# Kernel tuning notes

Measured on AMD Instinct MI355X. Metric: run time of the kernel, lower is better.

## Reference

```python
import jax, jax.numpy as jnp
import numpy as np

N, D, R, L, E, EP = 50000, 256, 16, 2, 300000, 100000
SCALING = 16.0 / 16.0  # alpha / rank


def _ln(x, g, b, eps=1e-5):
    mu = x.mean(-1, keepdims=True)
    var = ((x - mu) ** 2).mean(-1, keepdims=True)
    return (x - mu) * jax.lax.rsqrt(var + eps) * g + b


def setup_inputs() -> dict:
    key = jax.random.key(0)
    ks = iter(jax.random.split(key, 32))
    f = lambda shp, s=0.05: jax.random.normal(next(ks), shp, jnp.float32) * s
    return dict(
        x=f((2, N, D), 1.0),
        W_in=f((2, D, D)), b_in=f((2, D)),
        lora_A=f((2, R, D)), lora_B=f((2, D, R), 0.01),
        pn_g=jnp.ones((2, D), jnp.float32), pn_b=jnp.zeros((2, D), jnp.float32),
        W_self=f((L, 2, D, D)), W_neigh=f((L, 2, D, D)), b_sage=f((L, 2, D)),
        ln_g=jnp.ones((L, 2, D), jnp.float32), ln_b=jnp.zeros((L, 2, D), jnp.float32),
        Wv=f((2, D, D)), bv=f((2, D)), Wo=f((2, D, D)), bo=f((2, D)),
        e_src=jax.random.randint(next(ks), (2, E), 0, N, jnp.int32),
        e_dst=jax.random.randint(next(ks), (2, E), 0, N, jnp.int32),
        pos_src=jax.random.randint(next(ks), (EP,), 0, N, jnp.int32),
        pos_dst=jax.random.randint(next(ks), (EP,), 0, N, jnp.int32),
        neg_src=jax.random.randint(next(ks), (EP,), 0, N, jnp.int32),
        neg_dst=jax.random.randint(next(ks), (EP,), 0, N, jnp.int32),
    )


def reference(x, W_in, b_in, lora_A, lora_B, pn_g, pn_b, W_self, W_neigh,
              b_sage, ln_g, ln_b, Wv, bv, Wo, bo,
              e_src, e_dst, pos_src, pos_dst, neg_src, neg_dst):
    # ---- per-type input projection + LoRA adapter + patient LayerNorm ----
    base = jnp.einsum('tnd,tod->tno', x, W_in) + b_in[:, None]
    ad = jnp.einsum('tnr,tdr->tnd', jnp.einsum('tnd,trd->tnr', x, lora_A), lora_B) * SCALING
    h = _ln(base + ad, pn_g[:, None], pn_b[:, None])  # [2, N, D]

    def seg_mean(v, i):  # mean aggregation over incoming edges
        s = jax.ops.segment_sum(v, i, num_segments=N)
        c = jax.ops.segment_sum(jnp.ones((i.shape[0], 1), v.dtype), i, num_segments=N)
        return s / jnp.maximum(c, 1.0)

    # ---- SAGE layers over blocks (relation 0: a->b, relation 1: b->a) ----
    for i in range(L):
        msgs = jax.vmap(lambda hr, sr: hr[sr])(h, e_src)      # [2, E, D], src type r
        agg = jax.vmap(seg_mean)(msgs, e_dst)                 # agg[r] lands at dst type 1-r
        neigh = agg[::-1]                                     # neigh[t] for node type t
        h_new = (jnp.einsum('tnd,tod->tno', h, W_self[i])
                 + jnp.einsum('tnd,tod->tno', neigh, W_neigh[i])
                 + b_sage[i][:, None])
        if i == L - 1:
            # nn.MultiheadAttention with seq_len=1: softmax over 1 key == 1,
            # so attn_out = out_proj(v_proj(x)).
            v = jnp.einsum('tnd,tod->tno', h_new, Wv) + bv[:, None]
            h_new = jnp.einsum('tnd,tod->tno', v, Wo) + bo[:, None]
        if i > 0:
            h_new = h_new + h  # residual (shapes always match)
        h = _ln(h_new, ln_g[i][:, None], ln_b[i][:, None])
        # dropout is identity at inference

    # ---- dot-product edge predictor on pos/neg graphs for etype (a, rel, b) ----
    h_a, h_b = h[0], h[1]
    pos_score = jnp.sum(h_a[pos_src] * h_b[pos_dst], axis=-1)
    neg_score = jnp.sum(h_a[neg_src] * h_b[neg_dst], axis=-1)
    return pos_score, neg_score
```

## Files before the change

kernel.cpp:

```cpp
#include <hip/hip_runtime.h>

#define D 256
#define BK 64
#define SCAN_NB 64
#define SCAN_T (SCAN_NB * 256)

typedef __attribute__((ext_vector_type(8))) short bf16x8;
typedef __attribute__((ext_vector_type(4))) float f32x4;
typedef __attribute__((ext_vector_type(4))) unsigned int u32x4;

union frag_cvt { u32x4 u; bf16x8 h; };

__device__ __forceinline__ unsigned short bf16_rn(float f) {
    const unsigned int u = __float_as_uint(f);
    return (unsigned short)((u + 0x7FFFu + ((u >> 16) & 1u)) >> 16);
}
__device__ __forceinline__ float bf16_to_f32(unsigned short s) {
    return __uint_as_float(((unsigned int)s) << 16);
}

__global__ __launch_bounds__(256) void pre1_kernel(
    const float* __restrict__ W_in, const float* __restrict__ lA, const float* __restrict__ lB,
    unsigned short* __restrict__ win_eff,
    const float* __restrict__ W_self, unsigned short* __restrict__ ws0,
    const float* __restrict__ W_neigh, unsigned short* __restrict__ wn0,
    const float* __restrict__ Wo, const float* __restrict__ Wv, float* __restrict__ wvo,
    const float* __restrict__ bvp, const float* __restrict__ bo, float* __restrict__ bvo)
{
    const int b = blockIdx.x, tid = threadIdx.x;
    if (b < 512) {
        const int t = b >> 8, o = b & 255;
        float acc = W_in[((size_t)t * D + o) * D + tid];
        const float* Br = lB + ((size_t)t * D + o) * 16;
        const float* At = lA + (size_t)t * 16 * D;
        #pragma unroll
        for (int r = 0; r < 16; ++r) acc = fmaf(Br[r], At[r * D + tid], acc);
        win_eff[((size_t)t * D + o) * D + tid] = bf16_rn(acc);
    } else if (b < 1024) {
        const int i = (b - 512) * 256 + tid;
        ws0[i] = bf16_rn(W_self[i]);
    } else if (b < 1536) {
        const int i = (b - 1024) * 256 + tid;
        wn0[i] = bf16_rn(W_neigh[i]);
    } else if (b < 2048) {
        const int t = (b - 1536) >> 8, p = (b - 1536) & 255;
        const float* Xr = Wo + ((size_t)t * D + p) * D;
        const float* Yt = Wv + (size_t)t * D * D;
        float acc = 0.f;
        for (int o = 0; o < D; ++o) acc = fmaf(Xr[o], Yt[(size_t)o * D + tid], acc);
        wvo[((size_t)t * D + p) * D + tid] = acc;
    } else {
        const int t = b - 2048;
        const float* Mr = Wo + ((size_t)t * D + tid) * D;
        const float* vr = bvp + (size_t)t * D;
        float acc = bo[(size_t)t * D + tid];
        for (int o = 0; o < D; ++o) acc = fmaf(Mr[o], vr[o], acc);
        bvo[(size_t)t * D + tid] = acc;
    }
}

__global__ __launch_bounds__(256) void pre2_kernel(
    const float* __restrict__ wvo,
    const float* __restrict__ W_self1, unsigned short* __restrict__ ws1,
    const float* __restrict__ W_neigh1, unsigned short* __restrict__ wn1,
    const float* __restrict__ b_sage1, const float* __restrict__ bvo, float* __restrict__ b1e)
{
    const int b = blockIdx.x, tid = threadIdx.x;
    if (b < 512) {
        const int t = b >> 8, p = b & 255;
        const float* Xr = wvo + ((size_t)t * D + p) * D;
        const float* Yt = W_self1 + (size_t)t * D * D;
        float acc = 0.f;
        for (int o = 0; o < D; ++o) acc = fmaf(Xr[o], Yt[(size_t)o * D + tid], acc);
        ws1[((size_t)t * D + p) * D + tid] = bf16_rn(acc);
    } else if (b < 1024) {
        const int t = (b - 512) >> 8, p = (b - 512) & 255;
        const float* Xr = wvo + ((size_t)t * D + p) * D;
        const float* Yt = W_neigh1 + (size_t)t * D * D;
        float acc = 0.f;
        for (int o = 0; o < D; ++o) acc = fmaf(Xr[o], Yt[(size_t)o * D + tid], acc);
        wn1[((size_t)t * D + p) * D + tid] = bf16_rn(acc);
    } else {
        const int t = b - 1024;
        const float* Mr = wvo + ((size_t)t * D + tid) * D;
        const float* vr = b_sage1 + (size_t)t * D;
        float acc = bvo[(size_t)t * D + tid];
        for (int o = 0; o < D; ++o) acc = fmaf(Mr[o], vr[o], acc);
        b1e[(size_t)t * D + tid] = acc;
    }
}

__device__ __forceinline__ void load_bfrag(const unsigned short* __restrict__ Wp,
                                           int wn, int cidx, int rgrp,
                                           int kh, bf16x8 (&bq)[4][4])
{
    #pragma unroll
    for (int n = 0; n < 4; ++n) {
        const int o = wn + n * 16 + cidx;
        #pragma unroll
        for (int kk = 0; kk < 4; ++kk) {
            frag_cvt c;
            c.u = *(const u32x4*)(Wp + (size_t)o * D + kh * 128 + kk * 32 + rgrp * 8);
            bq[n][kk] = c.h;
        }
    }
}

__device__ __forceinline__ void gload_tile64(const unsigned short* __restrict__ Abase,
                                             int r0, int kt, int tid, char* lbuf)
{
    const int wbase = (tid >> 6) << 10;
    #pragma unroll
    for (int c = 0; c < 2; ++c) {
        const int p   = c * 4096 + tid * 16;
        const int row = p >> 7;
        const int lwb = p & 127;
        const int lg  = lwb ^ ((row & 7) << 4);
        const unsigned short* g = Abase + (size_t)(r0 + row) * D + kt + (lg >> 1);
        char* l = lbuf + c * 4096 + wbase;
        __builtin_amdgcn_global_load_lds(
            (const __attribute__((address_space(1))) unsigned int*)g,
            (__attribute__((address_space(3))) unsigned int*)l, 16, 0, 0);
    }
}

__device__ __forceinline__ void ln_epilogue(
    f32x4 (&acc)[4][4], unsigned short* SH,
    const float* __restrict__ bias, const unsigned short* __restrict__ res_bf,
    const float* __restrict__ g, const float* __restrict__ b,
    unsigned short* __restrict__ out_bf,
    int t, int m0, int M, int tid, int wid, int rgrp, int cidx, int wn)
{
    #pragma unroll
    for (int n = 0; n < 4; ++n) {
        const float bc = bias[t * D + wn + n * 16 + cidx];
        #pragma unroll
        for (int m = 0; m < 4; ++m)
            #pragma unroll
            for (int i = 0; i < 4; ++i)
                acc[m][n][i] += bc;
    }
    if (res_bf) {
        #pragma unroll
        for (int m = 0; m < 4; ++m)
            #pragma unroll
            for (int i = 0; i < 4; ++i) {
                const int row = m * 16 + rgrp * 4 + i;
                const int gr  = min(m0 + row, M - 1);
                const unsigned short* rr = res_bf + ((size_t)t * M + gr) * D + wn + cidx;
                #pragma unroll
                for (int n = 0; n < 4; ++n)
                    acc[m][n][i] += bf16_to_f32(rr[n * 16]);
            }
    }
    float* red  = (float*)((char*)SH + 16384);
    float* red2 = red + 256;
    float mu[4][4], rs[4][4];
    #pragma unroll
    for (int m = 0; m < 4; ++m)
        #pragma unroll
        for (int i = 0; i < 4; ++i) {
            float s = 0.f;
            #pragma unroll
            for (int n = 0; n < 4; ++n) s += acc[m][n][i];
            s += __shfl_xor(s, 1); s += __shfl_xor(s, 2);
            s += __shfl_xor(s, 4); s += __shfl_xor(s, 8);
            if (cidx == 0) red[(m * 16 + rgrp * 4 + i) * 4 + wid] = s;
        }
    __syncthreads();
    #pragma unroll
    for (int m = 0; m < 4; ++m)
        #pragma unroll
        for (int i = 0; i < 4; ++i) {
            const int row = m * 16 + rgrp * 4 + i;
            mu[m][i] = (red[row * 4] + red[row * 4 + 1] +
                        red[row * 4 + 2] + red[row * 4 + 3]) * (1.0f / 256.0f);
            float q = 0.f;
            #pragma unroll
            for (int n = 0; n < 4; ++n) {
                const float d0 = acc[m][n][i] - mu[m][i];
                q += d0 * d0;
            }
            q += __shfl_xor(q, 1); q += __shfl_xor(q, 2);
            q += __shfl_xor(q, 4); q += __shfl_xor(q, 8);
            if (cidx == 0) red2[row * 4 + wid] = q;
        }
    __syncthreads();
    #pragma unroll
    for (int m = 0; m < 4; ++m)
        #pragma unroll
        for (int i = 0; i < 4; ++i) {
            const int row = m * 16 + rgrp * 4 + i;
            rs[m][i] = rsqrtf((red2[row * 4] + red2[row * 4 + 1] +
                               red2[row * 4 + 2] + red2[row * 4 + 3]) * (1.0f / 256.0f) + 1e-5f);
        }
    __syncthreads();
    #pragma unroll
    for (int n = 0; n < 4; ++n) {
        const int col = wn + n * 16 + cidx;
        const float gv = g[t * D + col];
        const float bv = b[t * D + col];
        #pragma unroll
        for (int m = 0; m < 4; ++m)
            #pragma unroll
            for (int i = 0; i < 4; ++i) {
                const int row = m * 16 + rgrp * 4 + i;
                SH[row * 264 + col] = bf16_rn((acc[m][n][i] - mu[m][i]) * rs[m][i] * gv + bv);
            }
    }
    __syncthreads();
    unsigned short* Ct = out_bf + (size_t)t * M * D;
    #pragma unroll
    for (int it = 0; it < 8; ++it) {
        const int gidx = tid + it * 256;
        const int row  = gidx >> 5;
        const int cg   = gidx & 31;
        const int grow = m0 + row;
        if (grow < M) {
            const u32x4 v = *(const u32x4*)&SH[row * 264 + cg * 8];
            *(u32x4*)(Ct + (size_t)grow * D + cg * 8) = v;
        }
    }
}

__global__ __launch_bounds__(256, 2) void gemm_ln_kernel(
    const unsigned short* __restrict__ A, const unsigned short* __restrict__ W1,
    const unsigned short* __restrict__ A2, const unsigned short* __restrict__ W2,
    const float* __restrict__ bias, const unsigned short* __restrict__ res_bf,
    const float* __restrict__ g, const float* __restrict__ b,
    unsigned short* __restrict__ out_bf, int M, int swap2)
{
    const int t   = blockIdx.z;
    const int m0  = blockIdx.x * 64;
    const int tid = threadIdx.x;
    const int lane = tid & 63;
    const int wid  = tid >> 6;
    const int wn = wid * 64;
    const int rgrp = lane >> 4;
    const int cidx = lane & 15;

    __shared__ __align__(16) unsigned short SH[64 * 264];
    char* AsB0 = (char*)SH;
    char* AsB1 = (char*)SH + 8192;

    const int t2 = swap2 ? (1 - t) : t;
    const unsigned short* Aps[2] = { A  + (size_t)t  * M * D, A2 + (size_t)t2 * M * D };
    const unsigned short* Wps[2] = { W1 + (size_t)t  * D * D, W2 + (size_t)t  * D * D };

    f32x4 acc[4][4];
    #pragma unroll
    for (int i = 0; i < 4; ++i)
        #pragma unroll
        for (int j = 0; j < 4; ++j)
            acc[i][j] = (f32x4){0.f, 0.f, 0.f, 0.f};

    bf16x8 bq[2][4][4];
    gload_tile64(Aps[0], m0, 0, tid, AsB0);
    load_bfrag(Wps[0], wn, cidx, rgrp, 0, bq[0]);

    #pragma unroll
    for (int idx = 0; idx < 8; ++idx) {
        __syncthreads();
        if (idx < 7)
            gload_tile64(Aps[(idx + 1) >> 2], m0, ((idx + 1) & 3) * BK, tid,
                         (idx & 1) ? AsB0 : AsB1);
        if ((idx & 1) == 1 && idx < 7) {
            const int nh = (idx >> 1) + 1;
            load_bfrag(Wps[nh >> 1], wn, cidx, rgrp, nh & 1, bq[nh & 1]);
        }
        const char* cb = (idx & 1) ? AsB1 : AsB0;
        const int half = idx >> 1;
        #pragma unroll
        for (int ks = 0; ks < 2; ++ks) {
            const int kb = ks * 64 + rgrp * 16;
            bf16x8 af[4];
            #pragma unroll
            for (int m = 0; m < 4; ++m) {
                const int row = m * 16 + cidx;
                const int sw  = (row * 128 + kb) ^ ((row & 7) << 4);
                frag_cvt c; c.u = *(const u32x4*)(cb + sw); af[m] = c.h;
            }
            #pragma unroll
            for (int m = 0; m < 4; ++m)
                #pragma unroll
                for (int n = 0; n < 4; ++n)
                    acc[m][n] = __builtin_amdgcn_mfma_f32_16x16x32_bf16(
                        af[m], bq[half & 1][n][(idx & 1) * 2 + ks], acc[m][n], 0, 0, 0);
        }
        __syncthreads();
    }

    ln_epilogue(acc, SH, bias, res_bf, g, b, out_bf, t, m0, M, tid, wid, rgrp, cidx, wn);
}

__global__ __launch_bounds__(256, 2) void gemm_ln_in_kernel(
    const float* __restrict__ X, const unsigned short* __restrict__ Wb,
    const float* __restrict__ bias,
    const float* __restrict__ g, const float* __restrict__ b,
    unsigned short* __restrict__ out_bf, int M)
{
    const int t   = blockIdx.z;
    const int m0  = blockIdx.x * 64;
    const int tid = threadIdx.x;
    const int lane = tid & 63;
    const int wid  = tid >> 6;
    const int wn = wid * 64;
    const int rgrp = lane >> 4;
    const int cidx = lane & 15;

    __shared__ __align__(16) unsigned short SH[64 * 264];
    char* AsB = (char*)SH;

    const float* Xp = X + (size_t)t * M * D;
    const unsigned short* Wp = Wb + (size_t)t * D * D;

    f32x4 acc[4][4];
    #pragma unroll
    for (int i = 0; i < 4; ++i)
        #pragma unroll
        for (int j = 0; j < 4; ++j)
            acc[i][j] = (f32x4){0.f, 0.f, 0.f, 0.f};

    bf16x8 bq[2][4][4];
    float4 xr0[2], xr1[2];
    #pragma unroll
    for (int it = 0; it < 2; ++it) {
        const int gi = tid + it * 256;
        const int row = gi >> 3;
        const int kg = gi & 7;
        const int ar = min(m0 + row, M - 1);
        xr0[it] = *(const float4*)(Xp + (size_t)ar * D + kg * 8);
        xr1[it] = *(const float4*)(Xp + (size_t)ar * D + kg * 8 + 4);
    }
    load_bfrag(Wp, wn, cidx, rgrp, 0, bq[0]);

    #pragma unroll
    for (int kt_i = 0; kt_i < 4; ++kt_i) {
        #pragma unroll
        for (int it = 0; it < 2; ++it) {
            const int gi = tid + it * 256;
            const int row = gi >> 3;
            const int kg = gi & 7;
            unsigned int w[4];
            w[0] = ((unsigned int)bf16_rn(xr0[it].y) << 16) | bf16_rn(xr0[it].x);
            w[1] = ((unsigned int)bf16_rn(xr0[it].w) << 16) | bf16_rn(xr0[it].z);
            w[2] = ((unsigned int)bf16_rn(xr1[it].y) << 16) | bf16_rn(xr1[it].x);
            w[3] = ((unsigned int)bf16_rn(xr1[it].w) << 16) | bf16_rn(xr1[it].z);
            const int sw = ((row * BK + kg * 8) * 2) ^ ((row & 7) << 4);
            *(u32x4*)(AsB + sw) = (u32x4){w[0], w[1], w[2], w[3]};
        }
        __syncthreads();
        if (kt_i < 3) {
            const int kt = (kt_i + 1) * BK;
            #pragma unroll
            for (int it = 0; it < 2; ++it) {
                const int gi = tid + it * 256;
                const int row = gi >> 3;
                const int kg = gi & 7;
                const int ar = min(m0 + row, M - 1);
                xr0[it] = *(const float4*)(Xp + (size_t)ar * D + kt + kg * 8);
                xr1[it] = *(const float4*)(Xp + (size_t)ar * D + kt + kg * 8 + 4);
            }
        }
        if (kt_i == 1) load_bfrag(Wp, wn, cidx, rgrp, 1, bq[1]);
        #pragma unroll
        for (int ks = 0; ks < 2; ++ks) {
            const int kb = ks * 64 + rgrp * 16;
            bf16x8 af[4];
            #pragma unroll
            for (int m = 0; m < 4; ++m) {
                const int row = m * 16 + cidx;
                const int sw  = (row * 128 + kb) ^ ((row & 7) << 4);
                frag_cvt c; c.u = *(u32x4*)(AsB + sw); af[m] = c.h;
            }
            #pragma unroll
            for (int m = 0; m < 4; ++m)
                #pragma unroll
                for (int n = 0; n < 4; ++n)
                    acc[m][n] = __builtin_amdgcn_mfma_f32_16x16x32_bf16(
                        af[m], bq[kt_i >> 1][n][(kt_i & 1) * 2 + ks], acc[m][n], 0, 0, 0);
        }
        __syncthreads();
    }

    ln_epilogue(acc, SH, bias, nullptr, g, b, out_bf, t, m0, M, tid, wid, rgrp, cidx, wn);
}

__global__ void count_kernel(const int* __restrict__ e_dst, int* __restrict__ cnt,
                             int E2, int N, int E)
{
    const int i = blockIdx.x * 256 + threadIdx.x;
    if (i >= E2) return;
    const int t = i / E;
    atomicAdd(&cnt[(size_t)t * N + e_dst[i]], 1);
}

__global__ __launch_bounds__(256) void scan1_kernel(const int* __restrict__ cnt,
                                                    int* __restrict__ texcl,
                                                    int* __restrict__ bsum, int n, int c)
{
    __shared__ int ts[256];
    const int tid = threadIdx.x;
    const int gt  = blockIdx.x * 256 + tid;
    const int b   = gt * c;
    const int e   = min(b + c, n);
    int s = 0;
    for (int i = b; i < e; ++i) s += cnt[i];
    ts[tid] = s;
    __syncthreads();
    #pragma unroll
    for (int off = 1; off < 256; off <<= 1) {
        const int v = (tid >= off) ? ts[tid - off] : 0;
        __syncthreads();
        ts[tid] += v;
        __syncthreads();
    }
    texcl[gt] = ts[tid] - s;
    if (tid == 255) bsum[blockIdx.x] = ts[255];
}

__global__ __launch_bounds__(64) void scan2_kernel(int* __restrict__ bsum,
                                                   int* __restrict__ bbase,
                                                   int* __restrict__ offs, int n, int nb)
{
    const int lane = threadIdx.x;
    int v = (lane < nb) ? bsum[lane] : 0;
    int s = v;
    #pragma unroll
    for (int off = 1; off < 64; off <<= 1) {
        const int u = __shfl_up(s, off);
        if (lane >= off) s += u;
    }
    if (lane < nb) bbase[lane] = s - v;
    if (lane == 63) offs[n] = s;
}

__global__ __launch_bounds__(256) void scan3_kernel(const int* __restrict__ cnt,
                                                    const int* __restrict__ texcl,
                                                    const int* __restrict__ bbase,
                                                    int* __restrict__ offs, int n, int c)
{
    const int tid = threadIdx.x;
    const int gt  = blockIdx.x * 256 + tid;
    const int b   = gt * c;
    const int e   = min(b + c, n);
    int base = bbase[blockIdx.x] + texcl[gt];
    for (int i = b; i < e; ++i) { offs[i] = base; base += cnt[i]; }
}

__global__ void fill_kernel(const int* __restrict__ e_src, const int* __restrict__ e_dst,
                            const int* __restrict__ offs, int* __restrict__ cur,
                            int* __restrict__ sorted, int E2, int N, int E)
{
    const int i = blockIdx.x * 256 + threadIdx.x;
    if (i >= E2) return;
    const int t = i / E;
    const int idx = t * N + e_dst[i];
    const int pos = offs[idx] + atomicAdd(&cur[idx], 1);
    sorted[pos] = e_src[i];
}

__global__ __launch_bounds__(256) void agg_kernel(
    const unsigned short* __restrict__ hbf, const int* __restrict__ sorted_src,
    const int* __restrict__ offs, unsigned short* __restrict__ aggbf, int N)
{
    const int gw   = (blockIdx.x * 256 + threadIdx.x) >> 6;
    const int lane = threadIdx.x & 63;
    if (gw >= 2 * N) return;
    const int t = (gw >= N) ? 1 : 0;
    const int beg = offs[gw];
    const int end = offs[gw + 1];
    const unsigned short* hb = hbf + (size_t)t * N * D;
    float4 a0 = make_float4(0.f, 0.f, 0.f, 0.f);
    float4 a1 = make_float4(0.f, 0.f, 0.f, 0.f);
    int e = beg;
    for (; e + 2 <= end; e += 2) {
        const int s0 = sorted_src[e];
        const int s1 = sorted_src[e + 1];
        const ushort4 v0 = *(const ushort4*)(hb + (size_t)s0 * D + lane * 4);
        const ushort4 v1 = *(const ushort4*)(hb + (size_t)s1 * D + lane * 4);
        a0.x += bf16_to_f32(v0.x); a0.y += bf16_to_f32(v0.y);
        a0.z += bf16_to_f32(v0.z); a0.w += bf16_to_f32(v0.w);
        a1.x += bf16_to_f32(v1.x); a1.y += bf16_to_f32(v1.y);
        a1.z += bf16_to_f32(v1.z); a1.w += bf16_to_f32(v1.w);
    }
    if (e < end) {
        const int s0 = sorted_src[e];
        const ushort4 v0 = *(const ushort4*)(hb + (size_t)s0 * D + lane * 4);
        a0.x += bf16_to_f32(v0.x); a0.y += bf16_to_f32(v0.y);
        a0.z += bf16_to_f32(v0.z); a0.w += bf16_to_f32(v0.w);
    }
    const float inv = 1.0f / fmaxf((float)(end - beg), 1.0f);
    ushort4 o;
    o.x = bf16_rn((a0.x + a1.x) * inv); o.y = bf16_rn((a0.y + a1.y) * inv);
    o.z = bf16_rn((a0.z + a1.z) * inv); o.w = bf16_rn((a0.w + a1.w) * inv);
    *(ushort4*)(aggbf + (size_t)gw * D + lane * 4) = o;
}

__global__ __launch_bounds__(256) void score_kernel(
    const unsigned short* __restrict__ h,
    const int* __restrict__ pos_src, const int* __restrict__ pos_dst,
    const int* __restrict__ neg_src, const int* __restrict__ neg_dst,
    float* __restrict__ out, int EP, int N)
{
    const int wid  = (blockIdx.x * 256 + threadIdx.x) >> 6;
    const int lane = threadIdx.x & 63;
    if (wid >= 2 * EP) return;
    const int kind = wid / EP;
    const int k    = wid - kind * EP;
    const int s = kind ? neg_src[k] : pos_src[k];
    const int d = kind ? neg_dst[k] : pos_dst[k];
    const ushort4 a = *(const ushort4*)(h + (size_t)s * D + lane * 4);
    const ushort4 b = *(const ushort4*)(h + ((size_t)N + d) * D + lane * 4);
    float v = bf16_to_f32(a.x) * bf16_to_f32(b.x)
            + bf16_to_f32(a.y) * bf16_to_f32(b.y)
            + bf16_to_f32(a.z) * bf16_to_f32(b.z)
            + bf16_to_f32(a.w) * bf16_to_f32(b.w);
    #pragma unroll
    for (int off = 32; off > 0; off >>= 1) v += __shfl_down(v, off);
    if (lane == 0) out[wid] = v;
}

extern "C" void kernel_launch(void* const* d_in, const int* in_sizes, int n_in,
                              void* d_out, int out_size, void* d_ws, size_t ws_size,
                              hipStream_t stream)
{
    const float* x      = (const float*)d_in[0];
    const float* W_in   = (const float*)d_in[1];
    const float* b_in   = (const float*)d_in[2];
    const float* lora_A = (const float*)d_in[3];
    const float* lora_B = (const float*)d_in[4];
    const float* pn_g   = (const float*)d_in[5];
    const float* pn_b   = (const float*)d_in[6];
    const float* W_self = (const float*)d_in[7];
    const float* W_neigh= (const float*)d_in[8];
    const float* b_sage = (const float*)d_in[9];
    const float* ln_g   = (const float*)d_in[10];
    const float* ln_b   = (const float*)d_in[11];
    const float* Wv     = (const float*)d_in[12];
    const float* bvp    = (const float*)d_in[13];
    const float* Wo     = (const float*)d_in[14];
    const float* bo     = (const float*)d_in[15];
    const int* e_src    = (const int*)d_in[16];
    const int* e_dst    = (const int*)d_in[17];
    const int* pos_src  = (const int*)d_in[18];
    const int* pos_dst  = (const int*)d_in[19];
    const int* neg_src  = (const int*)d_in[20];
    const int* neg_dst  = (const int*)d_in[21];

    const int N  = in_sizes[0] / (2 * D);
    const int E  = in_sizes[16] / 2;
    const int EP = in_sizes[18];
    const size_t ND2 = (size_t)2 * N * D;
    const size_t DD2 = (size_t)2 * D * D;
    const int n2 = 2 * N;

    unsigned short* P0 = (unsigned short*)d_ws;
    unsigned short* P1 = P0 + ND2;
    unsigned short* P2 = P1 + ND2;
    unsigned short* T  = P2 + ND2;
    int* cnt    = (int*)(T + ND2);
    int* cur    = cnt + (size_t)n2;
    int* offs   = cur + (size_t)n2;
    int* sorted = offs + (size_t)n2 + 1;
    int* texcl  = sorted + (size_t)2 * E;
    int* bsum   = texcl + SCAN_T;
    int* bbase  = bsum + SCAN_NB;
    float* wvo  = (float*)(bbase + SCAN_NB);
    float* bvo  = wvo + DD2;
    float* b1e  = bvo + 2 * D;
    unsigned short* win_eff = (unsigned short*)(b1e + 2 * D);
    unsigned short* ws0 = win_eff + DD2;
    unsigned short* wn0 = ws0 + DD2;
    unsigned short* ws1 = wn0 + DD2;
    unsigned short* wn1 = ws1 + DD2;

    pre1_kernel<<<2050, 256, 0, stream>>>(W_in, lora_A, lora_B, win_eff,
                                          W_self, ws0, W_neigh, wn0,
                                          Wo, Wv, wvo, bvp, bo, bvo);
    pre2_kernel<<<1026, 256, 0, stream>>>(wvo, W_self + DD2, ws1,
                                          W_neigh + DD2, wn1,
                                          b_sage + 2 * D, bvo, b1e);

    hipMemsetAsync(cnt, 0, (size_t)2 * n2 * sizeof(int), stream);
    count_kernel<<<(2 * E + 255) / 256, 256, 0, stream>>>(e_dst, cnt, 2 * E, N, E);
    const int sc = (n2 + SCAN_T - 1) / SCAN_T;
    scan1_kernel<<<SCAN_NB, 256, 0, stream>>>(cnt, texcl, bsum, n2, sc);
    scan2_kernel<<<1, 64, 0, stream>>>(bsum, bbase, offs, n2, SCAN_NB);
    scan3_kernel<<<SCAN_NB, 256, 0, stream>>>(cnt, texcl, bbase, offs, n2, sc);
    fill_kernel<<<(2 * E + 255) / 256, 256, 0, stream>>>(e_src, e_dst, offs, cur, sorted, 2 * E, N, E);

    const dim3 gblk(256);
    const int mpan = (N + 63) / 64;
    const dim3 fgrid(mpan, 1, 2);

    gemm_ln_in_kernel<<<fgrid, gblk, 0, stream>>>(x, win_eff, b_in, pn_g, pn_b, P0, N);

    agg_kernel<<<dim3((2 * N + 3) / 4, 1, 1), gblk, 0, stream>>>(P0, sorted, offs, P1, N);
    gemm_ln_kernel<<<fgrid, gblk, 0, stream>>>(P0, ws0, P1, wn0, b_sage, nullptr,
                                               ln_g, ln_b, P2, N, 1);

    agg_kernel<<<dim3((2 * N + 3) / 4, 1, 1), gblk, 0, stream>>>(P2, sorted, offs, P1, N);
    gemm_ln_kernel<<<fgrid, gblk, 0, stream>>>(P2, ws1, P1, wn1, b1e, P2,
                                               ln_g + 2 * D, ln_b + 2 * D, P0, N, 1);

    score_kernel<<<(2 * EP + 3) / 4, gblk, 0, stream>>>(P0, pos_src, pos_dst, neg_src, neg_dst,
                                                        (float*)d_out, EP, N);
}
```

Before: 466.5 us.

## Single-pass LayerNorm stats, 4-way unrolled aggregation, half-wave score dot products

Three independent changes. The LayerNorm epilogue of gemm_ln_kernel now computes sum and sum of squares in one pass, which removes a shuffle round and one block barrier at the cost of the less stable E[x^2]-mu^2 variance form, clamped at zero. The neighbour aggregation loop is unrolled 4-way with four accumulators to keep more gathers in flight. The score kernel now handles two edge pairs per wavefront using 16-byte loads per lane, halving the grid size.

```diff
diff --git a/kernel.cpp b/kernel.cpp
--- a/kernel.cpp
+++ b/kernel.cpp
@@ -160,12 +160,21 @@
     for (int m = 0; m < 4; ++m)
         #pragma unroll
         for (int i = 0; i < 4; ++i) {
-            float s = 0.f;
-            #pragma unroll
-            for (int n = 0; n < 4; ++n) s += acc[m][n][i];
-            s += __shfl_xor(s, 1); s += __shfl_xor(s, 2);
-            s += __shfl_xor(s, 4); s += __shfl_xor(s, 8);
-            if (cidx == 0) red[(m * 16 + rgrp * 4 + i) * 4 + wid] = s;
+            float s = 0.f, q = 0.f;
+            #pragma unroll
+            for (int n = 0; n < 4; ++n) {
+                const float v = acc[m][n][i];
+                s += v; q += v * v;
+            }
+            s += __shfl_xor(s, 1); q += __shfl_xor(q, 1);
+            s += __shfl_xor(s, 2); q += __shfl_xor(q, 2);
+            s += __shfl_xor(s, 4); q += __shfl_xor(q, 4);
+            s += __shfl_xor(s, 8); q += __shfl_xor(q, 8);
+            if (cidx == 0) {
+                const int row = m * 16 + rgrp * 4 + i;
+                red[row * 4 + wid]  = s;
+                red2[row * 4 + wid] = q;
+            }
         }
     __syncthreads();
     #pragma unroll
@@ -173,26 +182,13 @@
         #pragma unroll
         for (int i = 0; i < 4; ++i) {
             const int row = m * 16 + rgrp * 4 + i;
-            mu[m][i] = (red[row * 4] + red[row * 4 + 1] +
-                        red[row * 4 + 2] + red[row * 4 + 3]) * (1.0f / 256.0f);
-            float q = 0.f;
-            #pragma unroll
-            for (int n = 0; n < 4; ++n) {
-                const float d0 = acc[m][n][i] - mu[m][i];
-                q += d0 * d0;
-            }
-            q += __shfl_xor(q, 1); q += __shfl_xor(q, 2);
-            q += __shfl_xor(q, 4); q += __shfl_xor(q, 8);
-            if (cidx == 0) red2[row * 4 + wid] = q;
-        }
-    __syncthreads();
-    #pragma unroll
-    for (int m = 0; m < 4; ++m)
-        #pragma unroll
-        for (int i = 0; i < 4; ++i) {
-            const int row = m * 16 + rgrp * 4 + i;
-            rs[m][i] = rsqrtf((red2[row * 4] + red2[row * 4 + 1] +
-                               red2[row * 4 + 2] + red2[row * 4 + 3]) * (1.0f / 256.0f) + 1e-5f);
+            const float S = red[row * 4] + red[row * 4 + 1] + red[row * 4 + 2] + red[row * 4 + 3];
+            const float Q = red2[row * 4] + red2[row * 4 + 1] + red2[row * 4 + 2] + red2[row * 4 + 3];
+            const float m_ = S * (1.0f / 256.0f);
+            float var = Q * (1.0f / 256.0f) - m_ * m_;
+            var = fmaxf(var, 0.f);
+            mu[m][i] = m_;
+            rs[m][i] = rsqrtf(var + 1e-5f);
         }
     __syncthreads();
     #pragma unroll
@@ -473,18 +469,28 @@
     const unsigned short* hb = hbf + (size_t)t * N * D;
     float4 a0 = make_float4(0.f, 0.f, 0.f, 0.f);
     float4 a1 = make_float4(0.f, 0.f, 0.f, 0.f);
+    float4 a2 = make_float4(0.f, 0.f, 0.f, 0.f);
+    float4 a3 = make_float4(0.f, 0.f, 0.f, 0.f);
     int e = beg;
-    for (; e + 2 <= end; e += 2) {
+    for (; e + 4 <= end; e += 4) {
         const int s0 = sorted_src[e];
         const int s1 = sorted_src[e + 1];
+        const int s2 = sorted_src[e + 2];
+        const int s3 = sorted_src[e + 3];
         const ushort4 v0 = *(const ushort4*)(hb + (size_t)s0 * D + lane * 4);
         const ushort4 v1 = *(const ushort4*)(hb + (size_t)s1 * D + lane * 4);
+        const ushort4 v2 = *(const ushort4*)(hb + (size_t)s2 * D + lane * 4);
+        const ushort4 v3 = *(const ushort4*)(hb + (size_t)s3 * D + lane * 4);
         a0.x += bf16_to_f32(v0.x); a0.y += bf16_to_f32(v0.y);
         a0.z += bf16_to_f32(v0.z); a0.w += bf16_to_f32(v0.w);
         a1.x += bf16_to_f32(v1.x); a1.y += bf16_to_f32(v1.y);
         a1.z += bf16_to_f32(v1.z); a1.w += bf16_to_f32(v1.w);
-    }
-    if (e < end) {
+        a2.x += bf16_to_f32(v2.x); a2.y += bf16_to_f32(v2.y);
+        a2.z += bf16_to_f32(v2.z); a2.w += bf16_to_f32(v2.w);
+        a3.x += bf16_to_f32(v3.x); a3.y += bf16_to_f32(v3.y);
+        a3.z += bf16_to_f32(v3.z); a3.w += bf16_to_f32(v3.w);
+    }
+    for (; e < end; ++e) {
         const int s0 = sorted_src[e];
         const ushort4 v0 = *(const ushort4*)(hb + (size_t)s0 * D + lane * 4);
         a0.x += bf16_to_f32(v0.x); a0.y += bf16_to_f32(v0.y);
@@ -492,8 +498,10 @@
     }
     const float inv = 1.0f / fmaxf((float)(end - beg), 1.0f);
     ushort4 o;
-    o.x = bf16_rn((a0.x + a1.x) * inv); o.y = bf16_rn((a0.y + a1.y) * inv);
-    o.z = bf16_rn((a0.z + a1.z) * inv); o.w = bf16_rn((a0.w + a1.w) * inv);
+    o.x = bf16_rn((a0.x + a1.x + a2.x + a3.x) * inv);
+    o.y = bf16_rn((a0.y + a1.y + a2.y + a3.y) * inv);
+    o.z = bf16_rn((a0.z + a1.z + a2.z + a3.z) * inv);
+    o.w = bf16_rn((a0.w + a1.w + a2.w + a3.w) * inv);
     *(ushort4*)(aggbf + (size_t)gw * D + lane * 4) = o;
 }
 
@@ -503,22 +511,31 @@
     const int* __restrict__ neg_src, const int* __restrict__ neg_dst,
     float* __restrict__ out, int EP, int N)
 {
-    const int wid  = (blockIdx.x * 256 + threadIdx.x) >> 6;
+    const int gw   = (blockIdx.x * 256 + threadIdx.x) >> 6;
     const int lane = threadIdx.x & 63;
-    if (wid >= 2 * EP) return;
-    const int kind = wid / EP;
-    const int k    = wid - kind * EP;
+    const int half = lane >> 5;
+    const int l32  = lane & 31;
+    const int pair = gw * 2 + half;
+    if (pair >= 2 * EP) return;
+    const int kind = pair / EP;
+    const int k    = pair - kind * EP;
     const int s = kind ? neg_src[k] : pos_src[k];
     const int d = kind ? neg_dst[k] : pos_dst[k];
-    const ushort4 a = *(const ushort4*)(h + (size_t)s * D + lane * 4);
-    const ushort4 b = *(const ushort4*)(h + ((size_t)N + d) * D + lane * 4);
-    float v = bf16_to_f32(a.x) * bf16_to_f32(b.x)
-            + bf16_to_f32(a.y) * bf16_to_f32(b.y)
-            + bf16_to_f32(a.z) * bf16_to_f32(b.z)
-            + bf16_to_f32(a.w) * bf16_to_f32(b.w);
-    #pragma unroll
-    for (int off = 32; off > 0; off >>= 1) v += __shfl_down(v, off);
-    if (lane == 0) out[wid] = v;
+    const u32x4 av = *(const u32x4*)(h + (size_t)s * D + l32 * 8);
+    const u32x4 bv = *(const u32x4*)(h + ((size_t)N + d) * D + l32 * 8);
+    float v = 0.f;
+    #pragma unroll
+    for (int j = 0; j < 4; ++j) {
+        const unsigned int ua = av[j], ub = bv[j];
+        v += __uint_as_float(ua << 16) * __uint_as_float(ub << 16);
+        v += __uint_as_float(ua & 0xFFFF0000u) * __uint_as_float(ub & 0xFFFF0000u);
+    }
+    v += __shfl_xor(v, 16);
+    v += __shfl_xor(v, 8);
+    v += __shfl_xor(v, 4);
+    v += __shfl_xor(v, 2);
+    v += __shfl_xor(v, 1);
+    if (l32 == 0) out[pair] = v;
 }
 
 extern "C" void kernel_launch(void* const* d_in, const int* in_sizes, int n_in,
@@ -604,6 +621,6 @@
     gemm_ln_kernel<<<fgrid, gblk, 0, stream>>>(P2, ws1, P1, wn1, b1e, P2,
                                                ln_g + 2 * D, ln_b + 2 * D, P0, N, 1);
 
-    score_kernel<<<(2 * EP + 3) / 4, gblk, 0, stream>>>(P0, pos_src, pos_dst, neg_src, neg_dst,
+    score_kernel<<<(2 * EP + 7) / 8, gblk, 0, stream>>>(P0, pos_src, pos_dst, neg_src, neg_dst,
                                                         (float*)d_out, EP, N);
 }
```

Measured after the change: 431.9 us. -7.4%, faster.
